# Performance work log

Measured on AMD Instinct MI355X. Metric: run time of the kernel, lower is better.

Reference implementation:

```python
import jax, jax.numpy as jnp
import numpy as np

E = 800000   # num edges
C = 64       # in_channels == out_channels
H = 4        # heads
D = C // H   # head_dim
N = 50000    # num_nodes


def setup_inputs() -> dict:
    key = jax.random.key(0)
    ks = jax.random.split(key, 10)
    s = 1.0 / np.sqrt(C)
    inp = {
        "query": jax.random.normal(ks[0], (E, C), jnp.float32),
        "key": jax.random.normal(ks[1], (E, C), jnp.float32),
        "value": jax.random.normal(ks[2], (E, C), jnp.float32),
        "Wq": jax.random.normal(ks[3], (C, C), jnp.float32) * s,
        "bq": jax.random.normal(ks[4], (C,), jnp.float32) * s,
        "Wk": jax.random.normal(ks[5], (C, C), jnp.float32) * s,
        "bk": jax.random.normal(ks[6], (C,), jnp.float32) * s,
        "Wv": jax.random.normal(ks[7], (C, C), jnp.float32) * s,
        "bv": jax.random.normal(ks[8], (C,), jnp.float32) * s,
        "index": jnp.sort(jax.random.randint(ks[9], (E,), 0, N, jnp.int32)),
        "num_nodes": N,
    }
    return inp


def reference(query, key, value, Wq, bq, Wk, bk, Wv, bv, index, num_nodes):
    # per-edge linear projections (groups=1 Linear)
    q = (query @ Wq + bq).reshape(E, H, D)
    k = (key @ Wk + bk).reshape(E, H, D)
    v = (value @ Wv + bv).reshape(E, H, D)

    # per-edge per-head scalar attention score
    score = jnp.einsum("ehd,ehd->eh", q, k) / jnp.sqrt(jnp.float32(D))  # [E, H]

    # restricted softmax over edges grouped by destination node (margin=0)
    smax = jax.ops.segment_max(score, index, num_segments=num_nodes)  # [N, H]
    smax = jnp.maximum(smax, 0.0)  # clamp(min=0); also fixes -inf on empty segments
    ex = jnp.exp(score - smax[index])                                  # [E, H]
    denom = jax.ops.segment_sum(ex, index, num_segments=num_nodes)    # [N, H]
    denom = denom + jnp.exp(-smax)                                     # margin - src_max with margin=0
    attn = ex / denom[index]                                           # [E, H]

    # weighted values (score is 1x1 per edge/head so this is a scale)
    out = attn[:, :, None] * v                                         # [E, H, D]
    return out.reshape(E, C)
```

## Files before the change

kernel.cpp:

```cpp
#include <hip/hip_runtime.h>
#include <hip/hip_bf16.h>
#include <math.h>

#define E_N 800000
#define C_N 64
#define H_N 4
#define D_N 16
#define NODES 50000

typedef __bf16 bf16x8 __attribute__((ext_vector_type(8)));
typedef float f32x4 __attribute__((ext_vector_type(4)));

__device__ __forceinline__ unsigned short f2bf_rne(float f) {
    unsigned int u = __float_as_uint(f);
    u += 0x7fffu + ((u >> 16) & 1u);
    return (unsigned short)(u >> 16);
}

union BfPack { bf16x8 v; unsigned short s[8]; };

__device__ __forceinline__ bf16x8 load_row_bf16(const float* __restrict__ p) {
    const float4* p4 = (const float4*)p;
    float4 a = p4[0], b = p4[1];
    BfPack u;
    u.s[0] = f2bf_rne(a.x); u.s[1] = f2bf_rne(a.y);
    u.s[2] = f2bf_rne(a.z); u.s[3] = f2bf_rne(a.w);
    u.s[4] = f2bf_rne(b.x); u.s[5] = f2bf_rne(b.y);
    u.s[6] = f2bf_rne(b.z); u.s[7] = f2bf_rne(b.w);
    return u.v;
}

__global__ void wt_kernel(const float* __restrict__ Wq,
                          const float* __restrict__ Wk,
                          const float* __restrict__ Wv,
                          unsigned short* __restrict__ wt) {
    int t = threadIdx.x;
    for (int w = 0; w < 3; ++w) {
        const float* W = (w == 0) ? Wq : (w == 1) ? Wk : Wv;
        for (int i = t; i < 4096; i += 256) {
            int o = i >> 6, c = i & 63;
            wt[w * 4096 + i] = f2bf_rne(W[c * 64 + o]);
        }
    }
}

__global__ __launch_bounds__(256) void score_kernel(
    const float* __restrict__ query, const float* __restrict__ key,
    const float* __restrict__ bq, const float* __restrict__ bk,
    const int* __restrict__ index,
    const unsigned short* __restrict__ wt,
    float* __restrict__ score, int* __restrict__ smax) {
    int lane = threadIdx.x & 63;
    int wid  = threadIdx.x >> 6;
    int e0   = blockIdx.x * 64 + wid * 16;
    int m    = lane & 15, quad = lane >> 4;

    const float* qrow = query + (size_t)(e0 + m) * 64 + quad * 8;
    const float* krow = key   + (size_t)(e0 + m) * 64 + quad * 8;
    bf16x8 aq0 = load_row_bf16(qrow);
    bf16x8 aq1 = load_row_bf16(qrow + 32);
    bf16x8 ak0 = load_row_bf16(krow);
    bf16x8 ak1 = load_row_bf16(krow + 32);

    const bf16x8* wq8 = (const bf16x8*)(wt);
    const bf16x8* wk8 = (const bf16x8*)(wt + 4096);

    int erel = lane >> 2;
    int hl   = lane & 3;
    int rw   = erel & 3;
    float s_mine = 0.f;

    #pragma unroll
    for (int h = 0; h < H_N; ++h) {
        int bi0 = (h * 16 + m) * 8 + quad;
        int bi1 = bi0 + 4;
        f32x4 cq = {0.f, 0.f, 0.f, 0.f}, ck = {0.f, 0.f, 0.f, 0.f};
        cq = __builtin_amdgcn_mfma_f32_16x16x32_bf16(aq0, wq8[bi0], cq, 0, 0, 0);
        cq = __builtin_amdgcn_mfma_f32_16x16x32_bf16(aq1, wq8[bi1], cq, 0, 0, 0);
        ck = __builtin_amdgcn_mfma_f32_16x16x32_bf16(ak0, wk8[bi0], ck, 0, 0, 0);
        ck = __builtin_amdgcn_mfma_f32_16x16x32_bf16(ak1, wk8[bi1], ck, 0, 0, 0);
        float bqv = bq[h * 16 + m], bkv = bk[h * 16 + m];
        float p[4];
        #pragma unroll
        for (int r = 0; r < 4; ++r) p[r] = (cq[r] + bqv) * (ck[r] + bkv);
        #pragma unroll
        for (int r = 0; r < 4; ++r) {
            p[r] += __shfl_xor(p[r], 1, 64);
            p[r] += __shfl_xor(p[r], 2, 64);
            p[r] += __shfl_xor(p[r], 4, 64);
            p[r] += __shfl_xor(p[r], 8, 64);
        }
        float pw = (rw == 0) ? p[0] : (rw == 1) ? p[1] : (rw == 2) ? p[2] : p[3];
        if (h == hl) s_mine = pw * 0.25f;
    }

    score[(size_t)e0 * 4 + lane] = s_mine;

    int e = e0 + erel;
    int n = index[e];
    float s = s_mine;
    #pragma unroll
    for (int d = 4; d <= 32; d <<= 1) {
        float up = __shfl_up(s, d, 64);
        int  nup = __shfl_up(n, d, 64);
        if (lane >= d && nup == n) s = fmaxf(s, up);
    }
    bool tail = (erel == 15) || (index[e + 1] != n);
    if (tail && s > 0.f)
        atomicMax(smax + n * 4 + hl, __float_as_int(s));
}

__global__ __launch_bounds__(256) void expsum_kernel(
    const float* __restrict__ score, const int* __restrict__ index,
    const int* __restrict__ smax, float* __restrict__ denom) {
    int lane = threadIdx.x & 63;
    int wid  = threadIdx.x >> 6;
    int e0   = blockIdx.x * 64 + wid * 16;
    int erel = lane >> 2, h = lane & 3;
    int e = e0 + erel;
    int n = index[e];
    float sm = __int_as_float(smax[n * 4 + h]);
    float s = __expf(score[(size_t)e0 * 4 + lane] - sm);
    #pragma unroll
    for (int d = 4; d <= 32; d <<= 1) {
        float up = __shfl_up(s, d, 64);
        int  nup = __shfl_up(n, d, 64);
        if (lane >= d && nup == n) s += up;
    }
    bool tail = (erel == 15) || (index[e + 1] != n);
    if (tail)
        atomicAdd(denom + n * 4 + h, s);
}

__global__ void finalize_kernel(const int* __restrict__ smax,
                                const float* __restrict__ denom,
                                float2* __restrict__ nd) {
    int i = blockIdx.x * 256 + threadIdx.x;
    if (i < NODES * H_N) {
        float sm = __int_as_float(smax[i]);
        float d  = denom[i] + __expf(-sm);
        nd[i] = make_float2(sm, 1.f / d);
    }
}

__global__ __launch_bounds__(256) void out_kernel(
    const float* __restrict__ value, const float* __restrict__ bv,
    const int* __restrict__ index, const unsigned short* __restrict__ wt,
    const float* __restrict__ score, const float2* __restrict__ nd,
    float* __restrict__ out) {
    int lane = threadIdx.x & 63;
    int wid  = threadIdx.x >> 6;
    int e0   = blockIdx.x * 64 + wid * 16;
    int m    = lane & 15, quad = lane >> 4;

    int erel = lane >> 2, hl = lane & 3;
    int n  = index[e0 + erel];
    float2 t = nd[n * 4 + hl];
    float attn = __expf(score[(size_t)e0 * 4 + lane] - t.x) * t.y;

    const float* vrow = value + (size_t)(e0 + m) * 64 + quad * 8;
    bf16x8 av0 = load_row_bf16(vrow);
    bf16x8 av1 = load_row_bf16(vrow + 32);
    const bf16x8* wv8 = (const bf16x8*)(wt + 8192);

    #pragma unroll
    for (int h = 0; h < H_N; ++h) {
        int bi0 = (h * 16 + m) * 8 + quad;
        f32x4 cv = {0.f, 0.f, 0.f, 0.f};
        cv = __builtin_amdgcn_mfma_f32_16x16x32_bf16(av0, wv8[bi0], cv, 0, 0, 0);
        cv = __builtin_amdgcn_mfma_f32_16x16x32_bf16(av1, wv8[bi0 + 4], cv, 0, 0, 0);
        float bvv = bv[h * 16 + m];
        #pragma unroll
        for (int r = 0; r < 4; ++r) {
            int row = quad * 4 + r;
            float a = __shfl(attn, (row << 2) | h, 64);
            out[(size_t)(e0 + row) * 64 + h * 16 + m] = (cv[r] + bvv) * a;
        }
    }
}

extern "C" void kernel_launch(void* const* d_in, const int* in_sizes, int n_in,
                              void* d_out, int out_size, void* d_ws, size_t ws_size,
                              hipStream_t stream) {
    const float* query = (const float*)d_in[0];
    const float* key   = (const float*)d_in[1];
    const float* value = (const float*)d_in[2];
    const float* Wq    = (const float*)d_in[3];
    const float* bq    = (const float*)d_in[4];
    const float* Wk    = (const float*)d_in[5];
    const float* bk    = (const float*)d_in[6];
    const float* Wv    = (const float*)d_in[7];
    const float* bv    = (const float*)d_in[8];
    const int*   index = (const int*)d_in[9];

    char* ws = (char*)d_ws;
    unsigned short* wt = (unsigned short*)ws;
    float* score = (float*)(ws + 32768);
    char*  p2    = ws + 32768 + (size_t)E_N * 16;
    int*   smax  = (int*)p2;
    float* denom = (float*)(p2 + (size_t)NODES * 16);
    float2* nd   = (float2*)(p2 + 2 * (size_t)NODES * 16);

    hipMemsetAsync(smax, 0, 2 * (size_t)NODES * 16, stream);
    wt_kernel<<<1, 256, 0, stream>>>(Wq, Wk, Wv, wt);
    score_kernel<<<E_N / 64, 256, 0, stream>>>(query, key, bq, bk, index, wt,
                                               score, smax);
    expsum_kernel<<<E_N / 64, 256, 0, stream>>>(score, index, smax, denom);
    finalize_kernel<<<(NODES * H_N + 255) / 256, 256, 0, stream>>>(smax, denom, nd);
    out_kernel<<<E_N / 64, 256, 0, stream>>>(value, bv, index, wt, score, nd,
                                             (float*)d_out);
}
```

Baseline: 672.9 us.

## Transpose MFMA operands so each lane holds an edge row; vectorize stores and expsum

Swaps the A/B operands of the bf16 MFMAs so the accumulator is laid out with edges along lanes and output channels along registers. The per-head dot-product reduction then takes two cross-quad shuffles instead of sixteen, and the output is written as 16-byte vector stores per edge row instead of scattered scalar stores. The expsum kernel now gives each lane one edge with all four heads, using vector loads of score and smax, a 64-wide segmented scan and four atomics per tail. The aim is to cut shuffle count, reduce uncoalesced stores and cut atomic traffic, at the cost of more registers per lane in expsum.

```diff
diff --git a/kernel.cpp b/kernel.cpp
--- a/kernel.cpp
+++ b/kernel.cpp
@@ -10,6 +10,7 @@
 
 typedef __bf16 bf16x8 __attribute__((ext_vector_type(8)));
 typedef float f32x4 __attribute__((ext_vector_type(4)));
+typedef int i32x4 __attribute__((ext_vector_type(4)));
 
 __device__ __forceinline__ unsigned short f2bf_rne(float f) {
     unsigned int u = __float_as_uint(f);
@@ -55,6 +56,8 @@
     int e0   = blockIdx.x * 64 + wid * 16;
     int m    = lane & 15, quad = lane >> 4;
 
+    int n = index[e0 + m];
+
     const float* qrow = query + (size_t)(e0 + m) * 64 + quad * 8;
     const float* krow = key   + (size_t)(e0 + m) * 64 + quad * 8;
     bf16x8 aq0 = load_row_bf16(qrow);
@@ -64,10 +67,9 @@
 
     const bf16x8* wq8 = (const bf16x8*)(wt);
     const bf16x8* wk8 = (const bf16x8*)(wt + 4096);
-
-    int erel = lane >> 2;
-    int hl   = lane & 3;
-    int rw   = erel & 3;
+    const f32x4* bq4p = (const f32x4*)bq;
+    const f32x4* bk4p = (const f32x4*)bk;
+
     float s_mine = 0.f;
 
     #pragma unroll
@@ -75,39 +77,34 @@
         int bi0 = (h * 16 + m) * 8 + quad;
         int bi1 = bi0 + 4;
         f32x4 cq = {0.f, 0.f, 0.f, 0.f}, ck = {0.f, 0.f, 0.f, 0.f};
-        cq = __builtin_amdgcn_mfma_f32_16x16x32_bf16(aq0, wq8[bi0], cq, 0, 0, 0);
-        cq = __builtin_amdgcn_mfma_f32_16x16x32_bf16(aq1, wq8[bi1], cq, 0, 0, 0);
-        ck = __builtin_amdgcn_mfma_f32_16x16x32_bf16(ak0, wk8[bi0], ck, 0, 0, 0);
-        ck = __builtin_amdgcn_mfma_f32_16x16x32_bf16(ak1, wk8[bi1], ck, 0, 0, 0);
-        float bqv = bq[h * 16 + m], bkv = bk[h * 16 + m];
-        float p[4];
-        #pragma unroll
-        for (int r = 0; r < 4; ++r) p[r] = (cq[r] + bqv) * (ck[r] + bkv);
-        #pragma unroll
-        for (int r = 0; r < 4; ++r) {
-            p[r] += __shfl_xor(p[r], 1, 64);
-            p[r] += __shfl_xor(p[r], 2, 64);
-            p[r] += __shfl_xor(p[r], 4, 64);
-            p[r] += __shfl_xor(p[r], 8, 64);
-        }
-        float pw = (rw == 0) ? p[0] : (rw == 1) ? p[1] : (rw == 2) ? p[2] : p[3];
-        if (h == hl) s_mine = pw * 0.25f;
-    }
-
-    score[(size_t)e0 * 4 + lane] = s_mine;
-
-    int e = e0 + erel;
-    int n = index[e];
+        cq = __builtin_amdgcn_mfma_f32_16x16x32_bf16(wq8[bi0], aq0, cq, 0, 0, 0);
+        cq = __builtin_amdgcn_mfma_f32_16x16x32_bf16(wq8[bi1], aq1, cq, 0, 0, 0);
+        ck = __builtin_amdgcn_mfma_f32_16x16x32_bf16(wk8[bi0], ak0, ck, 0, 0, 0);
+        ck = __builtin_amdgcn_mfma_f32_16x16x32_bf16(wk8[bi1], ak1, ck, 0, 0, 0);
+        f32x4 bqv = bq4p[h * 4 + quad];
+        f32x4 bkv = bk4p[h * 4 + quad];
+        float p = 0.f;
+        #pragma unroll
+        for (int r = 0; r < 4; ++r)
+            p += (cq[r] + bqv[r]) * (ck[r] + bkv[r]);
+        p += __shfl_xor(p, 16, 64);
+        p += __shfl_xor(p, 32, 64);
+        if (h == quad) s_mine = p * 0.25f;
+    }
+
+    score[(size_t)e0 * 4 + m * 4 + quad] = s_mine;
+
     float s = s_mine;
     #pragma unroll
-    for (int d = 4; d <= 32; d <<= 1) {
+    for (int d = 1; d <= 8; d <<= 1) {
         float up = __shfl_up(s, d, 64);
         int  nup = __shfl_up(n, d, 64);
-        if (lane >= d && nup == n) s = fmaxf(s, up);
-    }
-    bool tail = (erel == 15) || (index[e + 1] != n);
+        if (m >= d && nup == n) s = fmaxf(s, up);
+    }
+    int ndn = __shfl_down(n, 1, 64);
+    bool tail = (m == 15) || (ndn != n);
     if (tail && s > 0.f)
-        atomicMax(smax + n * 4 + hl, __float_as_int(s));
+        atomicMax(smax + n * 4 + quad, __float_as_int(s));
 }
 
 __global__ __launch_bounds__(256) void expsum_kernel(
@@ -115,21 +112,33 @@
     const int* __restrict__ smax, float* __restrict__ denom) {
     int lane = threadIdx.x & 63;
     int wid  = threadIdx.x >> 6;
-    int e0   = blockIdx.x * 64 + wid * 16;
-    int erel = lane >> 2, h = lane & 3;
-    int e = e0 + erel;
+    int e    = blockIdx.x * 256 + wid * 64 + lane;
+
     int n = index[e];
-    float sm = __int_as_float(smax[n * 4 + h]);
-    float s = __expf(score[(size_t)e0 * 4 + lane] - sm);
-    #pragma unroll
-    for (int d = 4; d <= 32; d <<= 1) {
-        float up = __shfl_up(s, d, 64);
-        int  nup = __shfl_up(n, d, 64);
-        if (lane >= d && nup == n) s += up;
-    }
-    bool tail = (erel == 15) || (index[e + 1] != n);
-    if (tail)
-        atomicAdd(denom + n * 4 + h, s);
+    i32x4 sm = ((const i32x4*)smax)[n];
+    f32x4 sc = ((const f32x4*)score)[e];
+    float ex[4];
+    #pragma unroll
+    for (int h = 0; h < 4; ++h)
+        ex[h] = __expf(sc[h] - __int_as_float(sm[h]));
+
+    #pragma unroll
+    for (int d = 1; d <= 32; d <<= 1) {
+        int nup = __shfl_up(n, d, 64);
+        bool ok = (lane >= d) && (nup == n);
+        #pragma unroll
+        for (int h = 0; h < 4; ++h) {
+            float up = __shfl_up(ex[h], d, 64);
+            if (ok) ex[h] += up;
+        }
+    }
+    int ndn = __shfl_down(n, 1, 64);
+    bool tail = (lane == 63) || (ndn != n);
+    if (tail) {
+        #pragma unroll
+        for (int h = 0; h < 4; ++h)
+            atomicAdd(denom + n * 4 + h, ex[h]);
+    }
 }
 
 __global__ void finalize_kernel(const int* __restrict__ smax,
@@ -153,29 +162,28 @@
     int e0   = blockIdx.x * 64 + wid * 16;
     int m    = lane & 15, quad = lane >> 4;
 
-    int erel = lane >> 2, hl = lane & 3;
-    int n  = index[e0 + erel];
-    float2 t = nd[n * 4 + hl];
-    float attn = __expf(score[(size_t)e0 * 4 + lane] - t.x) * t.y;
+    int n  = index[e0 + m];
+    float2 t = nd[n * 4 + quad];
+    float attn = __expf(score[(size_t)e0 * 4 + m * 4 + quad] - t.x) * t.y;
 
     const float* vrow = value + (size_t)(e0 + m) * 64 + quad * 8;
     bf16x8 av0 = load_row_bf16(vrow);
     bf16x8 av1 = load_row_bf16(vrow + 32);
     const bf16x8* wv8 = (const bf16x8*)(wt + 8192);
+    const f32x4* bv4p = (const f32x4*)bv;
 
     #pragma unroll
     for (int h = 0; h < H_N; ++h) {
         int bi0 = (h * 16 + m) * 8 + quad;
         f32x4 cv = {0.f, 0.f, 0.f, 0.f};
-        cv = __builtin_amdgcn_mfma_f32_16x16x32_bf16(av0, wv8[bi0], cv, 0, 0, 0);
-        cv = __builtin_amdgcn_mfma_f32_16x16x32_bf16(av1, wv8[bi0 + 4], cv, 0, 0, 0);
-        float bvv = bv[h * 16 + m];
-        #pragma unroll
-        for (int r = 0; r < 4; ++r) {
-            int row = quad * 4 + r;
-            float a = __shfl(attn, (row << 2) | h, 64);
-            out[(size_t)(e0 + row) * 64 + h * 16 + m] = (cv[r] + bvv) * a;
-        }
+        cv = __builtin_amdgcn_mfma_f32_16x16x32_bf16(wv8[bi0], av0, cv, 0, 0, 0);
+        cv = __builtin_amdgcn_mfma_f32_16x16x32_bf16(wv8[bi0 + 4], av1, cv, 0, 0, 0);
+        f32x4 bvv = bv4p[h * 4 + quad];
+        float a = __shfl(attn, (h << 4) | m, 64);
+        f32x4 o;
+        #pragma unroll
+        for (int r = 0; r < 4; ++r) o[r] = (cv[r] + bvv[r]) * a;
+        *(f32x4*)(out + (size_t)(e0 + m) * 64 + h * 16 + quad * 4) = o;
     }
 }
 
@@ -205,7 +213,7 @@
     wt_kernel<<<1, 256, 0, stream>>>(Wq, Wk, Wv, wt);
     score_kernel<<<E_N / 64, 256, 0, stream>>>(query, key, bq, bk, index, wt,
                                                score, smax);
-    expsum_kernel<<<E_N / 64, 256, 0, stream>>>(score, index, smax, denom);
+    expsum_kernel<<<E_N / 256, 256, 0, stream>>>(score, index, smax, denom);
     finalize_kernel<<<(NODES * H_N + 255) / 256, 256, 0, stream>>>(smax, denom, nd);
     out_kernel<<<E_N / 64, 256, 0, stream>>>(value, bv, index, wt, score, nd,
                                              (float*)d_out);
```

Measured after the change: 679.8 us. About the same (+1.0%).
